# Performance work log

Measured on AMD Instinct MI355X. Metric: run time of the kernel, lower is better.

## Reference

```python
import jax, jax.numpy as jnp
import numpy as np

N = 8192
DIM_IN = 1024
DIM_INNER = 1024
DIM_OUT = 1024


def setup_inputs() -> dict:
    key = jax.random.key(0)
    k1, k2, k3, k4 = jax.random.split(key, 4)
    x = jax.random.normal(k1, (N, DIM_IN), dtype=jnp.float32)
    # torch nn.Linear weights, stored transposed for right-multiplication
    Wqkv = jax.random.normal(k2, (DIM_IN, 3 * DIM_INNER), dtype=jnp.float32) * (DIM_IN ** -0.5)
    Wout = jax.random.normal(k3, (DIM_INNER, DIM_OUT), dtype=jnp.float32) * (DIM_INNER ** -0.5)
    bout = jax.random.normal(k4, (DIM_OUT,), dtype=jnp.float32) * 0.01
    return {"x": x, "Wqkv": Wqkv, "Wout": Wout, "bout": bout}


def reference(x, Wqkv, Wout, bout):
    scale = DIM_INNER ** -0.5
    qkv = x @ Wqkv                      # [N, 3*Di]
    q, k, v = jnp.split(qkv, 3, axis=-1)  # each [N, Di]
    sim = jnp.einsum('id,jd->ij', q, k) * scale  # [N, N]
    # causal mask: future positions (j > i) filled with -finfo.max
    i = jnp.arange(sim.shape[0])[:, None]
    j = jnp.arange(sim.shape[1])[None, :]
    sim = jnp.where(j > i, -jnp.finfo(sim.dtype).max, sim)
    attn = jax.nn.softmax(sim, axis=-1)
    out = jnp.einsum('ij,jd->id', attn, v)  # [N, Di]
    return out @ Wout + bout            # [N, Do]
```

## Files before the change

### kernel.cpp

```cpp
#include <hip/hip_runtime.h>
#include <hip/hip_bf16.h>


typedef __bf16 v8bf __attribute__((ext_vector_type(8)));
typedef float  v4f  __attribute__((ext_vector_type(4)));

struct __align__(8) S4 { short x, y, z, w; };

__device__ inline short f2bf(float f) {
  __hip_bfloat16 h = __float2bfloat16(f);
  return *reinterpret_cast<short*>(&h);
}
__device__ inline float bf2f(short s) {
  unsigned u = ((unsigned)(unsigned short)s) << 16;
  float f;
  __builtin_memcpy(&f, &u, 4);
  return f;
}

__device__ inline void stage_tile(const short* gbase, int ldg, short* lds, int tid) {
#pragma unroll
  for (int p = 0; p < 2; ++p) {
    const int c = p * 256 + tid;
    const int pos = (c & 3) ^ ((c >> 3) & 3);
    const short* g = gbase + (size_t)(c >> 2) * ldg + pos * 8;
    short* l = lds + p * 2048 + (tid >> 6) * 512;
    __builtin_amdgcn_global_load_lds(
        (__attribute__((address_space(1))) void*)(void*)g,
        (__attribute__((address_space(3))) void*)l, 16, 0, 0);
  }
}

__device__ inline void mma_step(const short* As, const short* Bs, v4f acc[4][4],
                                int lane, int wm, int wn) {
  const int qd = lane >> 4, r16 = lane & 15;
  const int sw = (qd ^ ((r16 >> 1) & 3)) * 8;
  const short* ab = As + (wm * 64 + r16) * 32 + sw;
  const short* bb = Bs + (wn * 64 + r16) * 32 + sw;
  v8bf a[4], b[4];
#pragma unroll
  for (int t = 0; t < 4; ++t) {
    a[t] = *(const v8bf*)(ab + t * 512);
    b[t] = *(const v8bf*)(bb + t * 512);
  }
#pragma unroll
  for (int mt = 0; mt < 4; ++mt)
#pragma unroll
    for (int nt = 0; nt < 4; ++nt)
      acc[mt][nt] = __builtin_amdgcn_mfma_f32_16x16x32_bf16(a[mt], b[nt], acc[mt][nt], 0, 0, 0);
}

#define ACC_INIT(acc)                              \
  _Pragma("unroll") for (int i_ = 0; i_ < 4; ++i_) \
  _Pragma("unroll") for (int j_ = 0; j_ < 4; ++j_) \
      acc[i_][j_] = (v4f){0.f, 0.f, 0.f, 0.f};

__global__ __launch_bounds__(256) void k_zerof(float* __restrict__ p, int n) {
  const int i = blockIdx.x * 256 + threadIdx.x;
  if (i < n) p[i] = 0.f;
}

__global__ __launch_bounds__(256) void k_detect(const unsigned short* __restrict__ xs,
                                                int* __restrict__ flag) {
  __shared__ int cnt;
  if (threadIdx.x == 0) cnt = 0;
  __syncthreads();
  int local = 0;
  for (int i = threadIdx.x; i < 4096; i += 256) {
    const unsigned e = (xs[i] >> 7) & 0xFFu;
    if (e >= 0xC0u) ++local;
  }
  if (local) atomicAdd(&cnt, local);
  __syncthreads();
  if (threadIdx.x == 0) *flag = (cnt > 8) ? 1 : 0;
}

__global__ __launch_bounds__(256) void k_convert(const void* __restrict__ in,
                                                 short* __restrict__ out, int n,
                                                 const int* __restrict__ flag) {
  const int stride = gridDim.x * blockDim.x;
  int i = blockIdx.x * blockDim.x + threadIdx.x;
  if (*flag != 0) {
    const float* p = (const float*)in;
    for (; i < n; i += stride) out[i] = f2bf(p[i]);
  } else {
    const short* p = (const short*)in;
    for (; i < n; i += stride) out[i] = p[i];
  }
}

__global__ __launch_bounds__(256) void k_to_f32(const void* __restrict__ in,
                                                float* __restrict__ out, int n,
                                                const int* __restrict__ flag) {
  const int stride = gridDim.x * blockDim.x;
  int i = blockIdx.x * blockDim.x + threadIdx.x;
  if (*flag != 0) {
    const float* p = (const float*)in;
    for (; i < n; i += stride) out[i] = p[i];
  } else {
    const short* p = (const short*)in;
    for (; i < n; i += stride) out[i] = bf2f(p[i]);
  }
}

__global__ __launch_bounds__(256) void k_convT(const void* __restrict__ in,
                                               short* __restrict__ out, int R, int C,
                                               const int* __restrict__ flag) {
  __shared__ short t[32][33];
  const int xx = threadIdx.x & 31, y0 = threadIdx.x >> 5;
  const int c0 = blockIdx.x * 32, r0 = blockIdx.y * 32;
  if (*flag != 0) {
    const float* p = (const float*)in;
#pragma unroll
    for (int i = 0; i < 4; ++i) {
      int r = y0 + i * 8;
      t[r][xx] = f2bf(p[(size_t)(r0 + r) * C + c0 + xx]);
    }
  } else {
    const short* p = (const short*)in;
#pragma unroll
    for (int i = 0; i < 4; ++i) {
      int r = y0 + i * 8;
      t[r][xx] = p[(size_t)(r0 + r) * C + c0 + xx];
    }
  }
  __syncthreads();
#pragma unroll
  for (int i = 0; i < 4; ++i) {
    int r = y0 + i * 8;
    out[(size_t)(c0 + r) * R + r0 + xx] = t[xx][r];
  }
}

__global__ __launch_bounds__(256) void k_gemm_qkv(const short* __restrict__ x,
                                                  const short* __restrict__ wt,
                                                  short* __restrict__ qk,
                                                  short* __restrict__ vT) {
  __shared__ short As[2][4096], Bs[2][4096];
  const int tid = threadIdx.x, lane = tid & 63, wave = tid >> 6;
  const int wm = wave >> 1, wn = wave & 1;
  const int lin = (int)blockIdx.y * 64 + (int)blockIdx.x;
  const int swz = (lin & 7) * 192 + (lin >> 3);
  const int m0 = (swz / 24) * 128, n0 = (swz % 24) * 128;
  const short* srcA = x + (size_t)m0 * 1024;
  const short* srcB = wt + (size_t)n0 * 1024;
  v4f acc[4][4];
  ACC_INIT(acc)
  stage_tile(srcA, 1024, As[0], tid);
  stage_tile(srcB, 1024, Bs[0], tid);
  __syncthreads();
  for (int k0 = 0; k0 < 1024; k0 += 32) {
    const int cur = (k0 >> 5) & 1;
    if (k0 + 32 < 1024) {
      stage_tile(srcA + k0 + 32, 1024, As[cur ^ 1], tid);
      stage_tile(srcB + k0 + 32, 1024, Bs[cur ^ 1], tid);
    }
    mma_step(As[cur], Bs[cur], acc, lane, wm, wn);
    __syncthreads();
  }
  const int qd = lane >> 4, c16 = lane & 15;
#pragma unroll
  for (int mt = 0; mt < 4; ++mt) {
    const int rl = wm * 64 + mt * 16 + qd * 4;
#pragma unroll
    for (int nt = 0; nt < 4; ++nt) {
      const int cl = wn * 64 + nt * 16 + c16;
      const int n = n0 + cl;
      if (n < 2048) {
#pragma unroll
        for (int r = 0; r < 4; ++r)
          qk[(size_t)(m0 + rl + r) * 2048 + n] = f2bf(acc[mt][nt][r]);
      } else {
        S4 p;
        p.x = f2bf(acc[mt][nt][0]);
        p.y = f2bf(acc[mt][nt][1]);
        p.z = f2bf(acc[mt][nt][2]);
        p.w = f2bf(acc[mt][nt][3]);
        *reinterpret_cast<S4*>(vT + (size_t)(n - 2048) * 8192 + (m0 + rl)) = p;
      }
    }
  }
}

__global__ __launch_bounds__(256) void k_qk_exp(const short* __restrict__ qk,
                                                short* __restrict__ E,
                                                float* __restrict__ l) {
  __shared__ short As[2][4096], Bs[2][4096];
  __shared__ float srow[128][2];
  const int tid = threadIdx.x, lane = tid & 63, wave = tid >> 6;
  const int wm = wave >> 1, wn = wave & 1;
  const int b = ((int)blockIdx.x & 7) * 260 + ((int)blockIdx.x >> 3);
  int I = (int)((sqrtf(8.f * (float)b + 1.f) - 1.f) * 0.5f);
  while ((I + 1) * (I + 2) / 2 <= b) ++I;
  while (I * (I + 1) / 2 > b) --I;
  const int J = b - I * (I + 1) / 2;
  const int m0 = I * 128, n0 = J * 128;
  const short* srcA = qk + (size_t)m0 * 2048;
  const short* srcB = qk + 1024 + (size_t)n0 * 2048;
  v4f acc[4][4];
  ACC_INIT(acc)
  stage_tile(srcA, 2048, As[0], tid);
  stage_tile(srcB, 2048, Bs[0], tid);
  __syncthreads();
  for (int k0 = 0; k0 < 1024; k0 += 32) {
    const int cur = (k0 >> 5) & 1;
    if (k0 + 32 < 1024) {
      stage_tile(srcA + k0 + 32, 2048, As[cur ^ 1], tid);
      stage_tile(srcB + k0 + 32, 2048, Bs[cur ^ 1], tid);
    }
    mma_step(As[cur], Bs[cur], acc, lane, wm, wn);
    __syncthreads();
  }
  short* tb = E + (size_t)(I * (I + 1) / 2 + J) * 16384;
  const int qd = lane >> 4, c16 = lane & 15;
  float rp[4][4];
#pragma unroll
  for (int mt = 0; mt < 4; ++mt)
#pragma unroll
    for (int r = 0; r < 4; ++r) rp[mt][r] = 0.f;
#pragma unroll
  for (int mt = 0; mt < 4; ++mt) {
    const int rl = wm * 64 + mt * 16 + qd * 4;
#pragma unroll
    for (int nt = 0; nt < 4; ++nt) {
      const int cl = wn * 64 + nt * 16 + c16;
      const int gj = n0 + cl;
      const int jj = cl >> 5, qdc = (cl >> 3) & 3, jl = cl & 7;
      short* dst = tb + (((wm * 4 + jj) * 4 + mt) * 512) + qdc * 128 + jl;
#pragma unroll
      for (int r = 0; r < 4; ++r) {
        const int gi = m0 + rl + r;
        const float s = fminf(acc[mt][nt][r] * 0.03125f, 60.f);
        const float e = (gj > gi) ? 0.f : __expf(s);
        dst[(qd * 4 + r) * 8] = f2bf(e);
        rp[mt][r] += e;
      }
    }
  }
#pragma unroll
  for (int mt = 0; mt < 4; ++mt)
#pragma unroll
    for (int r = 0; r < 4; ++r) {
      float v = rp[mt][r];
      v += __shfl_xor(v, 1);
      v += __shfl_xor(v, 2);
      v += __shfl_xor(v, 4);
      v += __shfl_xor(v, 8);
      rp[mt][r] = v;
    }
  if ((lane & 15) == 0) {
#pragma unroll
    for (int mt = 0; mt < 4; ++mt)
#pragma unroll
      for (int r = 0; r < 4; ++r)
        srow[wm * 64 + mt * 16 + qd * 4 + r][wn] = rp[mt][r];
  }
  __syncthreads();
  if (tid < 128) atomicAdd(&l[m0 + tid], srow[tid][0] + srow[tid][1]);
}

__device__ __forceinline__ void pv_loadA8(v8bf a[4], const short* __restrict__ Et,
                                          int wave, int lane) {
  const int wm_ = wave >> 2, mt_ = wave & 3;
#pragma unroll
  for (int jj = 0; jj < 4; ++jj) {
    const int BLK = (wm_ * 4 + jj) * 4 + mt_;
    a[jj] = *(const v8bf*)(Et + BLK * 512 + lane * 8);
  }
}

__device__ __forceinline__ void pv_stageV8(const short* __restrict__ vbJ,
                                           short* __restrict__ lds, int tid) {
#pragma unroll
  for (int p = 0; p < 4; ++p) {
    const int c = p * 512 + tid;
    const int row = c >> 4;
    const int kc = (c & 15) ^ (row & 15);
    const short* g = vbJ + (size_t)row * 8192 + kc * 8;
    short* lp = lds + (p * 512 + (tid >> 6) * 64) * 8;
    __builtin_amdgcn_global_load_lds(
        (__attribute__((address_space(1))) void*)(void*)g,
        (__attribute__((address_space(3))) void*)lp, 16, 0, 0);
  }
}

__device__ __forceinline__ void pv_compute8(const v8bf a[4], const short* __restrict__ Vbuf,
                                            v4f acc[8], int qd, int r16) {
#pragma unroll
  for (int jj = 0; jj < 4; ++jj) {
    v8bf b[8];
#pragma unroll
    for (int u = 0; u < 8; ++u) {
      const int row = u * 16 + r16;
      const int kc = (jj * 4 + qd) ^ r16;
      b[u] = *(const v8bf*)(Vbuf + row * 128 + kc * 8);
    }
#pragma unroll
    for (int u = 0; u < 8; ++u)
      acc[u] = __builtin_amdgcn_mfma_f32_16x16x32_bf16(a[jj], b[u], acc[u], 0, 0, 0);
  }
}

__global__ __launch_bounds__(512) void k_pv(const short* __restrict__ E,
                                            const short* __restrict__ vT,
                                            const float* __restrict__ l,
                                            short* __restrict__ attn) {
  __shared__ short Vb[2][16384];
  const int tid = threadIdx.x, lane = tid & 63, wave = tid >> 6;
  const int bx = (int)blockIdx.x;
  const int n0 = (int)blockIdx.y * 128;
  const int qd = lane >> 4, r16 = lane & 15;
  const short* vb = vT + (size_t)n0 * 8192;
  for (int half = 0; half < 2; ++half) {
    const int I = half ? 63 - bx : bx;
    const int m0 = I * 128;
    const short* Erow = E + (size_t)(I * (I + 1) / 2) * 16384;
    v4f acc[8];
#pragma unroll
    for (int u = 0; u < 8; ++u) acc[u] = (v4f){0.f, 0.f, 0.f, 0.f};
    v8bf aA[4], aB[4];
    __syncthreads();
    pv_stageV8(vb, Vb[0], tid);
    pv_loadA8(aA, Erow, wave, lane);
    __syncthreads();
    for (int J = 0;; J += 2) {
      if (J + 1 <= I) {
        pv_loadA8(aB, Erow + (size_t)(J + 1) * 16384, wave, lane);
        pv_stageV8(vb + (J + 1) * 128, Vb[1], tid);
      }
      pv_compute8(aA, Vb[0], acc, qd, r16);
      if (J + 1 > I) break;
      __syncthreads();
      if (J + 2 <= I) {
        pv_loadA8(aA, Erow + (size_t)(J + 2) * 16384, wave, lane);
        pv_stageV8(vb + (J + 2) * 128, Vb[0], tid);
      }
      pv_compute8(aB, Vb[1], acc, qd, r16);
      if (J + 2 > I) break;
      __syncthreads();
    }
    const int rbase = wave * 16 + qd * 4;
    float inv[4];
#pragma unroll
    for (int r = 0; r < 4; ++r) inv[r] = 1.0f / fmaxf(l[m0 + rbase + r], 1e-30f);
#pragma unroll
    for (int u = 0; u < 8; ++u) {
#pragma unroll
      for (int r = 0; r < 4; ++r)
        attn[(size_t)(m0 + rbase + r) * 1024 + n0 + u * 16 + r16] = f2bf(acc[u][r] * inv[r]);
    }
  }
}

__global__ __launch_bounds__(256) void k_gemm_out(const short* __restrict__ attn,
                                                  const short* __restrict__ wt,
                                                  const float* __restrict__ bout,
                                                  float* __restrict__ out) {
  __shared__ short As[2][4096], Bs[2][4096];
  const int tid = threadIdx.x, lane = tid & 63, wave = tid >> 6;
  const int wm = wave >> 1, wn = wave & 1;
  const int lin = (int)blockIdx.y * 64 + (int)blockIdx.x;
  const int swz = (lin & 7) * 64 + (lin >> 3);
  const int m0 = (swz >> 3) * 128, n0 = (swz & 7) * 128;
  const short* srcA = attn + (size_t)m0 * 1024;
  const short* srcB = wt + (size_t)n0 * 1024;
  v4f acc[4][4];
  ACC_INIT(acc)
  stage_tile(srcA, 1024, As[0], tid);
  stage_tile(srcB, 1024, Bs[0], tid);
  __syncthreads();
  for (int k0 = 0; k0 < 1024; k0 += 32) {
    const int cur = (k0 >> 5) & 1;
    if (k0 + 32 < 1024) {
      stage_tile(srcA + k0 + 32, 1024, As[cur ^ 1], tid);
      stage_tile(srcB + k0 + 32, 1024, Bs[cur ^ 1], tid);
    }
    mma_step(As[cur], Bs[cur], acc, lane, wm, wn);
    __syncthreads();
  }
  const int qd = lane >> 4, c16 = lane & 15;
#pragma unroll
  for (int mt = 0; mt < 4; ++mt) {
    const int rl = wm * 64 + mt * 16 + qd * 4;
#pragma unroll
    for (int nt = 0; nt < 4; ++nt) {
      const int cl = wn * 64 + nt * 16 + c16;
      const float bias = bout[n0 + cl];
#pragma unroll
      for (int r = 0; r < 4; ++r)
        out[(size_t)(m0 + rl + r) * 1024 + n0 + cl] = acc[mt][nt][r] + bias;
    }
  }
}

extern "C" void kernel_launch(void* const* d_in, const int* in_sizes, int n_in,
                              void* d_out, int out_size, void* d_ws, size_t ws_size,
                              hipStream_t stream) {
  (void)out_size; (void)ws_size;
  const void *x = d_in[0], *Wqkv = d_in[1], *Wout = d_in[2], *bout = d_in[3];
  for (int i = 0; i < n_in; ++i) {
    switch (in_sizes[i]) {
      case 8192 * 1024: x = d_in[i]; break;
      case 1024 * 3072: Wqkv = d_in[i]; break;
      case 1024 * 1024: Wout = d_in[i]; break;
      case 1024:        bout = d_in[i]; break;
      default: break;
    }
  }

  char* ws = (char*)d_ws;
  short* qk    = (short*)(ws);
  short* vT    = (short*)(ws + 33554432);
  short* E     = (short*)(ws + 50331648);
  short* xb    = (short*)(ws + 118489088);
  short* attn  = xb;
  short* WqT   = (short*)(ws + 135266304);
  short* WoT   = (short*)(ws + 141557760);
  float* boutf = (float*)(ws + 143654912);
  float* lsum  = (float*)(ws + 143659008);
  int*   flag  = (int*)  (ws + 143691776);

  k_detect<<<1, 256, 0, stream>>>((const unsigned short*)x, flag);
  k_zerof<<<32, 256, 0, stream>>>(lsum, 8192);
  k_convert<<<1024, 256, 0, stream>>>(x, xb, 8192 * 1024, flag);
  k_to_f32<<<1, 256, 0, stream>>>(bout, boutf, 1024, flag);
  k_convT<<<dim3(96, 32), 256, 0, stream>>>(Wqkv, WqT, 1024, 3072, flag);
  k_convT<<<dim3(32, 32), 256, 0, stream>>>(Wout, WoT, 1024, 1024, flag);
  k_gemm_qkv<<<dim3(64, 24), 256, 0, stream>>>(xb, WqT, qk, vT);
  k_qk_exp<<<dim3(2080), 256, 0, stream>>>(qk, E, lsum);
  k_pv<<<dim3(32, 8), 512, 0, stream>>>(E, vT, lsum, attn);
  k_gemm_out<<<dim3(64, 8), 256, 0, stream>>>(attn, WoT, boutf, (float*)d_out);
}
```

Before: 402.6 us.

## Triple-buffer GEMM tiles with explicit vmcnt waits and single barrier

Converts the three GEMM-style kernels from a double-buffered LDS pipeline to a triple-buffered one that keeps two tile loads in flight. Each stage waits on a partial vmcnt and issues one barrier instead of a full drain plus a sync. The PV kernel now issues the V staging before the E fragment loads. This raises LDS use per block to 48KB, which may lower occupancy, and it relies on stage_tile issuing exactly four outstanding global-to-LDS ops per tile pair for the vmcnt(4) to be correct.

New measurement: 453.8 us. 1.13x slower.

```diff
diff --git a/kernel.cpp b/kernel.cpp
--- a/kernel.cpp
+++ b/kernel.cpp
@@ -6,6 +6,10 @@
 typedef float  v4f  __attribute__((ext_vector_type(4)));
 
 struct __align__(8) S4 { short x, y, z, w; };
+
+#define VMCNT4() asm volatile("s_waitcnt vmcnt(4)" ::: "memory")
+#define VMCNT0() asm volatile("s_waitcnt vmcnt(0)" ::: "memory")
+#define BARRIER() do { __builtin_amdgcn_s_barrier(); asm volatile("" ::: "memory"); } while (0)
 
 __device__ inline short f2bf(float f) {
   __hip_bfloat16 h = __float2bfloat16(f);
@@ -136,7 +140,7 @@
                                                   const short* __restrict__ wt,
                                                   short* __restrict__ qk,
                                                   short* __restrict__ vT) {
-  __shared__ short As[2][4096], Bs[2][4096];
+  __shared__ short As[3][4096], Bs[3][4096];
   const int tid = threadIdx.x, lane = tid & 63, wave = tid >> 6;
   const int wm = wave >> 1, wn = wave & 1;
   const int lin = (int)blockIdx.y * 64 + (int)blockIdx.x;
@@ -148,16 +152,20 @@
   ACC_INIT(acc)
   stage_tile(srcA, 1024, As[0], tid);
   stage_tile(srcB, 1024, Bs[0], tid);
-  __syncthreads();
-  for (int k0 = 0; k0 < 1024; k0 += 32) {
-    const int cur = (k0 >> 5) & 1;
-    if (k0 + 32 < 1024) {
-      stage_tile(srcA + k0 + 32, 1024, As[cur ^ 1], tid);
-      stage_tile(srcB + k0 + 32, 1024, Bs[cur ^ 1], tid);
-    }
-    mma_step(As[cur], Bs[cur], acc, lane, wm, wn);
-    __syncthreads();
-  }
+  stage_tile(srcA + 32, 1024, As[1], tid);
+  stage_tile(srcB + 32, 1024, Bs[1], tid);
+  for (int t = 0; t < 31; ++t) {
+    VMCNT4();
+    BARRIER();
+    if (t < 30) {
+      stage_tile(srcA + (t + 2) * 32, 1024, As[(t + 2) % 3], tid);
+      stage_tile(srcB + (t + 2) * 32, 1024, Bs[(t + 2) % 3], tid);
+    }
+    mma_step(As[t % 3], Bs[t % 3], acc, lane, wm, wn);
+  }
+  VMCNT0();
+  BARRIER();
+  mma_step(As[31 % 3], Bs[31 % 3], acc, lane, wm, wn);
   const int qd = lane >> 4, c16 = lane & 15;
 #pragma unroll
   for (int mt = 0; mt < 4; ++mt) {
@@ -185,7 +193,7 @@
 __global__ __launch_bounds__(256) void k_qk_exp(const short* __restrict__ qk,
                                                 short* __restrict__ E,
                                                 float* __restrict__ l) {
-  __shared__ short As[2][4096], Bs[2][4096];
+  __shared__ short As[3][4096], Bs[3][4096];
   __shared__ float srow[128][2];
   const int tid = threadIdx.x, lane = tid & 63, wave = tid >> 6;
   const int wm = wave >> 1, wn = wave & 1;
@@ -201,16 +209,20 @@
   ACC_INIT(acc)
   stage_tile(srcA, 2048, As[0], tid);
   stage_tile(srcB, 2048, Bs[0], tid);
-  __syncthreads();
-  for (int k0 = 0; k0 < 1024; k0 += 32) {
-    const int cur = (k0 >> 5) & 1;
-    if (k0 + 32 < 1024) {
-      stage_tile(srcA + k0 + 32, 2048, As[cur ^ 1], tid);
-      stage_tile(srcB + k0 + 32, 2048, Bs[cur ^ 1], tid);
-    }
-    mma_step(As[cur], Bs[cur], acc, lane, wm, wn);
-    __syncthreads();
-  }
+  stage_tile(srcA + 32, 2048, As[1], tid);
+  stage_tile(srcB + 32, 2048, Bs[1], tid);
+  for (int t = 0; t < 31; ++t) {
+    VMCNT4();
+    BARRIER();
+    if (t < 30) {
+      stage_tile(srcA + (t + 2) * 32, 2048, As[(t + 2) % 3], tid);
+      stage_tile(srcB + (t + 2) * 32, 2048, Bs[(t + 2) % 3], tid);
+    }
+    mma_step(As[t % 3], Bs[t % 3], acc, lane, wm, wn);
+  }
+  VMCNT0();
+  BARRIER();
+  mma_step(As[31 % 3], Bs[31 % 3], acc, lane, wm, wn);
   short* tb = E + (size_t)(I * (I + 1) / 2 + J) * 16384;
   const int qd = lane >> 4, c16 = lane & 15;
   float rp[4][4];
@@ -325,15 +337,15 @@
     __syncthreads();
     for (int J = 0;; J += 2) {
       if (J + 1 <= I) {
+        pv_stageV8(vb + (J + 1) * 128, Vb[1], tid);
         pv_loadA8(aB, Erow + (size_t)(J + 1) * 16384, wave, lane);
-        pv_stageV8(vb + (J + 1) * 128, Vb[1], tid);
       }
       pv_compute8(aA, Vb[0], acc, qd, r16);
       if (J + 1 > I) break;
       __syncthreads();
       if (J + 2 <= I) {
+        pv_stageV8(vb + (J + 2) * 128, Vb[0], tid);
         pv_loadA8(aA, Erow + (size_t)(J + 2) * 16384, wave, lane);
-        pv_stageV8(vb + (J + 2) * 128, Vb[0], tid);
       }
       pv_compute8(aB, Vb[1], acc, qd, r16);
       if (J + 2 > I) break;
@@ -356,7 +368,7 @@
                                                   const short* __restrict__ wt,
                                                   const float* __restrict__ bout,
                                                   float* __restrict__ out) {
-  __shared__ short As[2][4096], Bs[2][4096];
+  __shared__ short As[3][4096], Bs[3][4096];
   const int tid = threadIdx.x, lane = tid & 63, wave = tid >> 6;
   const int wm = wave >> 1, wn = wave & 1;
   const int lin = (int)blockIdx.y * 64 + (int)blockIdx.x;
@@ -368,16 +380,20 @@
   ACC_INIT(acc)
   stage_tile(srcA, 1024, As[0], tid);
   stage_tile(srcB, 1024, Bs[0], tid);
-  __syncthreads();
-  for (int k0 = 0; k0 < 1024; k0 += 32) {
-    const int cur = (k0 >> 5) & 1;
-    if (k0 + 32 < 1024) {
-      stage_tile(srcA + k0 + 32, 1024, As[cur ^ 1], tid);
-      stage_tile(srcB + k0 + 32, 1024, Bs[cur ^ 1], tid);
-    }
-    mma_step(As[cur], Bs[cur], acc, lane, wm, wn);
-    __syncthreads();
-  }
+  stage_tile(srcA + 32, 1024, As[1], tid);
+  stage_tile(srcB + 32, 1024, Bs[1], tid);
+  for (int t = 0; t < 31; ++t) {
+    VMCNT4();
+    BARRIER();
+    if (t < 30) {
+      stage_tile(srcA + (t + 2) * 32, 1024, As[(t + 2) % 3], tid);
+      stage_tile(srcB + (t + 2) * 32, 1024, Bs[(t + 2) % 3], tid);
+    }
+    mma_step(As[t % 3], Bs[t % 3], acc, lane, wm, wn);
+  }
+  VMCNT0();
+  BARRIER();
+  mma_step(As[31 % 3], Bs[31 % 3], acc, lane, wm, wn);
   const int qd = lane >> 4, c16 = lane & 15;
 #pragma unroll
   for (int mt = 0; mt < 4; ++mt) {
```
